# Kernel tuning notes

Measured on AMD Instinct MI355X. Metric: run time of the kernel, lower is better.

## Reference

```python
import jax, jax.numpy as jnp
import numpy as np
from jax import lax


def setup_inputs() -> dict:
    key = jax.random.key(0)
    t_in = jax.random.normal(key, (16, 65536, 3), dtype=jnp.float32)
    return {"npoints": 2048, "t_in": t_in}


def reference(npoints, t_in):
    """Iterative farthest point sampling.

    t_in: (b, n, 3) float32 point coordinates.
    Returns (b, npoints) int32 indices of sampled points.
    Matches the PointNet++ CUDA kernel semantics: first sample is index 0,
    running min-distance buffer initialized to a large value, each step
    picks the argmax of the min-distance to the already-selected set.
    """
    b, n, p = t_in.shape
    assert p == 3
    BIG = jnp.float32(1e10)

    batch_ix = jnp.arange(b)

    def step(carry, _):
        dist, last_idx = carry                      # dist: (b,n), last_idx: (b,)
        last = t_in[batch_ix, last_idx]             # (b,3) last selected points
        d = jnp.sum((t_in - last[:, None, :]) ** 2, axis=-1)  # (b,n)
        dist = jnp.minimum(dist, d)
        nxt = jnp.argmax(dist, axis=-1).astype(jnp.int32)      # (b,)
        return (dist, nxt), nxt

    init_idx = jnp.zeros((b,), dtype=jnp.int32)
    dist0 = jnp.full((b, n), BIG, dtype=jnp.float32)
    (_, _), idxs = lax.scan(step, (dist0, init_idx), None, length=npoints - 1)
    # idxs: (npoints-1, b) -> (b, npoints-1)
    out = jnp.concatenate([init_idx[:, None], idxs.T], axis=1)  # (b, npoints)
    return out
```

## Files before the change

kernel.cpp:

```cpp
#include <hip/hip_runtime.h>
#include <stdint.h>


#define NBATCH   16
#define NPTS     65536
#define NPOINTS  2048
#define KBLK     16
#define THREADS  256
#define PPB      4096
#define PPT      16
#define QPB      4
#define SLOT_U64 2
#define REGION_U64 (KBLK * QPB * SLOT_U64)

#define TAGOK(w) (((unsigned)((w) >> 16) & 0xFFFFu) == tag)

typedef unsigned int uint4v __attribute__((ext_vector_type(4)));
typedef unsigned int uint2v __attribute__((ext_vector_type(2)));

__device__ __forceinline__ void load_slot16(const unsigned long long* p,
                                            unsigned long long& w0,
                                            unsigned long long& w1) {
    uint4v r;
    asm volatile("global_load_dwordx4 %0, %1, off sc1\n\t"
                 "s_waitcnt vmcnt(0)"
                 : "=v"(r) : "v"(p) : "memory");
    w0 = ((unsigned long long)r.y << 32) | r.x;
    w1 = ((unsigned long long)r.w << 32) | r.z;
}

__device__ __forceinline__ void red_combine(double& d, int& i,
                                            double od, int oi) {
    const bool t = (od > d) || (od == d && oi < i);
    d = t ? od : d; i = t ? oi : i;
}

template <int CTRL>
__device__ __forceinline__ void red_dpp(double& d, int& i) {
    const int hi = __double2hiint(d), lo = __double2loint(d);
    const int ohi = __builtin_amdgcn_update_dpp(hi, hi, CTRL, 0xF, 0xF, false);
    const int olo = __builtin_amdgcn_update_dpp(lo, lo, CTRL, 0xF, 0xF, false);
    const int oi  = __builtin_amdgcn_update_dpp(i,  i,  CTRL, 0xF, 0xF, false);
    red_combine(d, i, __hiloint2double(ohi, olo), oi);
}

__device__ __forceinline__ void red_swz16(double& d, int& i) {
    const int ohi = __builtin_amdgcn_ds_swizzle(__double2hiint(d), 0x401F);
    const int olo = __builtin_amdgcn_ds_swizzle(__double2loint(d), 0x401F);
    const int oi  = __builtin_amdgcn_ds_swizzle(i, 0x401F);
    red_combine(d, i, __hiloint2double(ohi, olo), oi);
}

__device__ __forceinline__ void red_x32(double& d, int& i, bool hi_half) {
    const unsigned hi = (unsigned)__double2hiint(d);
    const unsigned lo = (unsigned)__double2loint(d);
    uint2v rh = __builtin_amdgcn_permlane32_swap(hi, hi, false, false);
    uint2v rl = __builtin_amdgcn_permlane32_swap(lo, lo, false, false);
    uint2v ri = __builtin_amdgcn_permlane32_swap((unsigned)i, (unsigned)i,
                                                 false, false);
    const int ohi = (int)(hi_half ? rh[0] : rh[1]);
    const int olo = (int)(hi_half ? rl[0] : rl[1]);
    const int oi  = (int)(hi_half ? ri[0] : ri[1]);
    red_combine(d, i, __hiloint2double(ohi, olo), oi);
}

__device__ __forceinline__ void argmax64(double& d, int& i, bool hi_half) {
    red_dpp<0xB1>(d, i);
    red_dpp<0x4E>(d, i);
    red_dpp<0x141>(d, i);
    red_dpp<0x140>(d, i);
    red_swz16(d, i);
    red_x32(d, i, hi_half);
}

__global__ __launch_bounds__(THREADS, 1)
void fps_kernel(const float* __restrict__ pts, int* __restrict__ out,
                unsigned long long* __restrict__ slots)
{
    const int bid  = blockIdx.x;
    const int g    = bid & 15;
    const int blk  = bid >> 4;
    const int tid  = threadIdx.x;
    const int lane = tid & 63;
    const int wave = tid >> 6;
    const bool hi_half = (lane >= 32);

    const float* __restrict__ P = pts + (size_t)g * (NPTS * 3);

    __shared__ unsigned long long s_mail[2][4];

    double xd[PPT], yd[PPT], zd[PPT], dist[PPT];
    const int base = blk * PPB;
#pragma unroll
    for (int j = 0; j < PPT; ++j) {
        const int idx = base + j * THREADS + tid;
        xd[j] = (double)P[idx * 3 + 0];
        yd[j] = (double)P[idx * 3 + 1];
        zd[j] = (double)P[idx * 3 + 2];
        dist[j] = 1e10;
    }
    if (tid < 8) ((unsigned long long*)s_mail)[tid] = 0ull;
    __syncthreads();

    double qx = (double)P[0], qy = (double)P[1], qz = (double)P[2];
    if (blk == 0 && tid == 0) out[g * NPOINTS] = 0;

    for (int it = 0; it < NPOINTS - 1; ++it) {
        double bd = -1.0;
        int    bi = 0x7FFFFFFF;
        {
#pragma clang fp contract(off)
#pragma unroll
            for (int j = 0; j < PPT; ++j) {
                const double dx = xd[j] - qx;
                const double dy = yd[j] - qy;
                const double dz = zd[j] - qz;
                const double d  = (dx * dx + dy * dy) + dz * dz;
                const double nd = fmin(dist[j], d);
                dist[j] = nd;
                const bool t = nd > bd;
                bd = t ? nd : bd;
                bi = t ? (base + j * THREADS + tid) : bi;
            }
        }

        argmax64(bd, bi, hi_half);

        const unsigned tag = (unsigned)(it + 1);
        const int par = it & 1;
        unsigned long long* rb =
            slots + (size_t)(par * NBATCH + g) * REGION_U64;

        const unsigned long long B =
            (unsigned long long)__double_as_longlong(bd);
        const unsigned long long TI =
              ((unsigned long long)tag << 16)
            | (unsigned long long)((unsigned)bi & 0xFFFFu);
        const unsigned long long own0 = ((B >> 32) << 32) | TI;
        const unsigned long long own1 = ((B & 0xFFFFFFFFull) << 32) | TI;

        if (lane < 2) {
            __hip_atomic_store(rb + (blk * QPB + wave) * SLOT_U64 + lane,
                               (lane == 0) ? own0 : own1,
                               __ATOMIC_RELAXED,
                               __HIP_MEMORY_SCOPE_AGENT);
        }

        float qxf, qyf, qzf;

        if (wave != 0) {
            unsigned long long f1, f2, f3;
            int guard = 0;
            bool okm;
            do {
                f1 = __hip_atomic_load(&s_mail[par][0], __ATOMIC_RELAXED,
                                       __HIP_MEMORY_SCOPE_WORKGROUP);
                f2 = __hip_atomic_load(&s_mail[par][1], __ATOMIC_RELAXED,
                                       __HIP_MEMORY_SCOPE_WORKGROUP);
                f3 = __hip_atomic_load(&s_mail[par][2], __ATOMIC_RELAXED,
                                       __HIP_MEMORY_SCOPE_WORKGROUP);
                okm = ((unsigned)f1 == tag) & ((unsigned)f2 == tag)
                    & ((unsigned)f3 == tag);
            } while (!okm && ++guard < (1 << 20));
            qxf = __int_as_float((int)(f1 >> 32));
            qyf = __int_as_float((int)(f2 >> 32));
            qzf = __int_as_float((int)(f3 >> 32));
        } else {
            unsigned long long* sp = rb + lane * SLOT_U64;
            const bool own = (lane == blk * QPB);
            unsigned long long l0 = own0, l1 = own1;
            bool ok = own;
            __builtin_amdgcn_s_sleep(12);
            int g1 = 0;
            while (!ok && g1 < 32) {
                load_slot16(sp, l0, l1);
                ok = TAGOK(l0) & TAGOK(l1);
                ++g1;
            }
            int g2 = 0;
            while (!ok) {
                l0 = __hip_atomic_load(sp + 0, __ATOMIC_RELAXED,
                                       __HIP_MEMORY_SCOPE_AGENT);
                l1 = __hip_atomic_load(sp + 1, __ATOMIC_RELAXED,
                                       __HIP_MEMORY_SCOPE_AGENT);
                ok = TAGOK(l0) & TAGOK(l1);
                if (++g2 > (1 << 20)) break;
            }

            double cd = __longlong_as_double(
                (long long)(((l0 >> 32) << 32) | (l1 >> 32)));
            int    ci = (int)(l0 & 0xFFFFull);

            const int    si = ci;
            const float* pc = P + (size_t)(unsigned)si * 3;
            const float px = pc[0];
            const float py = pc[1];
            const float pz = pc[2];

            argmax64(cd, ci, hi_half);

            if (lane == 0 && blk == 0) out[g * NPOINTS + it + 1] = ci;

            const unsigned long long mb = __ballot(si == ci);
            const int wl = (__ffsll(mb) - 1) & 63;
            qxf = __int_as_float(
                __builtin_amdgcn_readlane(__float_as_int(px), wl));
            qyf = __int_as_float(
                __builtin_amdgcn_readlane(__float_as_int(py), wl));
            qzf = __int_as_float(
                __builtin_amdgcn_readlane(__float_as_int(pz), wl));

            if (lane < 3) {
                const unsigned coord =
                    (lane == 0) ? (unsigned)__float_as_int(qxf)
                  : (lane == 1) ? (unsigned)__float_as_int(qyf)
                                : (unsigned)__float_as_int(qzf);
                __hip_atomic_store(&s_mail[par][lane],
                                   ((unsigned long long)coord << 32)
                                 | (unsigned long long)tag,
                                   __ATOMIC_RELAXED,
                                   __HIP_MEMORY_SCOPE_WORKGROUP);
            }
        }

        qx = (double)qxf; qy = (double)qyf; qz = (double)qzf;
    }
}

extern "C" void kernel_launch(void* const* d_in, const int* in_sizes, int n_in,
                              void* d_out, int out_size, void* d_ws, size_t ws_size,
                              hipStream_t stream) {
    (void)in_sizes; (void)n_in; (void)out_size; (void)ws_size;
    const float* t_in = (const float*)d_in[1];
    int* out = (int*)d_out;
    unsigned long long* slots = (unsigned long long*)d_ws;

    dim3 grid(NBATCH * KBLK);
    dim3 block(THREADS);
    void* args[] = { (void*)&t_in, (void*)&out, (void*)&slots };
    hipLaunchCooperativeKernel((const void*)fps_kernel, grid, block, args, 0, stream);
}
```

Baseline: 4.301 ms.

## Publish winner coordinates in exchange slots and poll via pipelined global-to-LDS loads

Each wave now tracks the float coordinates of its local best point and publishes them, tag-protected, alongside distance and index in a wider 4-word slot. The exchange wave no longer has to gather the winning point's coordinates from global memory after the cross-block reduction. Polling switches from a serialized load-and-wait loop to four rounds of asynchronous global-to-LDS loads that stay in flight together, and slot writes now use atomic swap instructions. This takes a dependent global load off the per-iteration critical path and shortens polling latency, at the cost of extra registers, LDS buffers and more traffic per slot. The wide path is chosen only when the workspace is large enough, with the old path kept as a fallback.

Result: slower. 7.668 ms (+78.3%).

```diff
diff --git a/kernel.cpp b/kernel.cpp
--- a/kernel.cpp
+++ b/kernel.cpp
@@ -10,23 +10,25 @@
 #define PPB      4096
 #define PPT      16
 #define QPB      4
-#define SLOT_U64 2
-#define REGION_U64 (KBLK * QPB * SLOT_U64)
+#define SLOT_N   2
+#define REGION_N (KBLK * QPB * SLOT_N)
+#define SLOT_W   4
+#define REGION_W (KBLK * QPB * SLOT_W)
+#define WS_NEED_WIDE (2 * NBATCH * REGION_W * 8)
 
 #define TAGOK(w) (((unsigned)((w) >> 16) & 0xFFFFu) == tag)
 
 typedef unsigned int uint4v __attribute__((ext_vector_type(4)));
 typedef unsigned int uint2v __attribute__((ext_vector_type(2)));
-
-__device__ __forceinline__ void load_slot16(const unsigned long long* p,
-                                            unsigned long long& w0,
-                                            unsigned long long& w1) {
+typedef unsigned long long ull;
+
+__device__ __forceinline__ void load_slot16(const ull* p, ull& w0, ull& w1) {
     uint4v r;
     asm volatile("global_load_dwordx4 %0, %1, off sc1\n\t"
                  "s_waitcnt vmcnt(0)"
                  : "=v"(r) : "v"(p) : "memory");
-    w0 = ((unsigned long long)r.y << 32) | r.x;
-    w1 = ((unsigned long long)r.w << 32) | r.z;
+    w0 = ((ull)r.y << 32) | r.x;
+    w1 = ((ull)r.w << 32) | r.z;
 }
 
 __device__ __forceinline__ void red_combine(double& d, int& i,
@@ -73,9 +75,10 @@
     red_x32(d, i, hi_half);
 }
 
+template <int WIDE>
 __global__ __launch_bounds__(THREADS, 1)
 void fps_kernel(const float* __restrict__ pts, int* __restrict__ out,
-                unsigned long long* __restrict__ slots)
+                ull* __restrict__ slots)
 {
     const int bid  = blockIdx.x;
     const int g    = bid & 15;
@@ -87,19 +90,23 @@
 
     const float* __restrict__ P = pts + (size_t)g * (NPTS * 3);
 
-    __shared__ unsigned long long s_mail[2][4];
+    __shared__ ull s_mail[2][4];
+    __shared__ ull pbuf[4][2][64][2];
 
     double xd[PPT], yd[PPT], zd[PPT], dist[PPT];
+    float  xf[PPT], yf[PPT], zf[PPT];
     const int base = blk * PPB;
 #pragma unroll
     for (int j = 0; j < PPT; ++j) {
         const int idx = base + j * THREADS + tid;
-        xd[j] = (double)P[idx * 3 + 0];
-        yd[j] = (double)P[idx * 3 + 1];
-        zd[j] = (double)P[idx * 3 + 2];
+        const float a = P[idx * 3 + 0];
+        const float b = P[idx * 3 + 1];
+        const float c = P[idx * 3 + 2];
+        xd[j] = (double)a; yd[j] = (double)b; zd[j] = (double)c;
+        if (WIDE) { xf[j] = a; yf[j] = b; zf[j] = c; }
         dist[j] = 1e10;
     }
-    if (tid < 8) ((unsigned long long*)s_mail)[tid] = 0ull;
+    if (tid < 8) ((ull*)s_mail)[tid] = 0ull;
     __syncthreads();
 
     double qx = (double)P[0], qy = (double)P[1], qz = (double)P[2];
@@ -108,6 +115,7 @@
     for (int it = 0; it < NPOINTS - 1; ++it) {
         double bd = -1.0;
         int    bi = 0x7FFFFFFF;
+        float  bx = 0.f, by = 0.f, bz = 0.f;
         {
 #pragma clang fp contract(off)
 #pragma unroll
@@ -121,6 +129,11 @@
                 const bool t = nd > bd;
                 bd = t ? nd : bd;
                 bi = t ? (base + j * THREADS + tid) : bi;
+                if (WIDE) {
+                    bx = t ? xf[j] : bx;
+                    by = t ? yf[j] : by;
+                    bz = t ? zf[j] : bz;
+                }
             }
         }
 
@@ -128,28 +141,47 @@
 
         const unsigned tag = (unsigned)(it + 1);
         const int par = it & 1;
-        unsigned long long* rb =
-            slots + (size_t)(par * NBATCH + g) * REGION_U64;
-
-        const unsigned long long B =
-            (unsigned long long)__double_as_longlong(bd);
-        const unsigned long long TI =
-              ((unsigned long long)tag << 16)
-            | (unsigned long long)((unsigned)bi & 0xFFFFu);
-        const unsigned long long own0 = ((B >> 32) << 32) | TI;
-        const unsigned long long own1 = ((B & 0xFFFFFFFFull) << 32) | TI;
-
-        if (lane < 2) {
-            __hip_atomic_store(rb + (blk * QPB + wave) * SLOT_U64 + lane,
-                               (lane == 0) ? own0 : own1,
-                               __ATOMIC_RELAXED,
-                               __HIP_MEMORY_SCOPE_AGENT);
+        ull* rb = slots + (size_t)(par * NBATCH + g)
+                        * (WIDE ? REGION_W : REGION_N);
+
+        const ull B  = (ull)__double_as_longlong(bd);
+        const ull TI = ((ull)tag << 16) | (ull)((unsigned)bi & 0xFFFFu);
+        const ull own0 = ((B >> 32) << 32) | TI;
+        const ull own1 = ((B & 0xFFFFFFFFull) << 32) | TI;
+        ull own2 = 0, own3 = 0;
+        if (WIDE) {
+            const int src_lane = (bi - base) & 63;
+            const unsigned xw = (unsigned)__builtin_amdgcn_readlane(
+                                    __float_as_int(bx), src_lane);
+            const unsigned yw = (unsigned)__builtin_amdgcn_readlane(
+                                    __float_as_int(by), src_lane);
+            const unsigned zw = (unsigned)__builtin_amdgcn_readlane(
+                                    __float_as_int(bz), src_lane);
+            own2 = ((ull)xw << 32) | ((ull)tag << 16) | (ull)(yw >> 16);
+            own3 = ((ull)zw << 32) | ((ull)tag << 16) | (ull)(yw & 0xFFFFu);
         }
 
+        if (WIDE) {
+            if (lane < 4) {
+                ull* dst = rb + (blk * QPB + wave) * SLOT_W + lane;
+                const ull v = (lane == 0) ? own0 : (lane == 1) ? own1
+                            : (lane == 2) ? own2 : own3;
+                asm volatile("global_atomic_swap_x2 %0, %1, off"
+                             :: "v"(dst), "v"(v) : "memory");
+            }
+        } else {
+            if (lane < 2) {
+                ull* dst = rb + (blk * QPB + wave) * SLOT_N + lane;
+                const ull v = (lane == 0) ? own0 : own1;
+                asm volatile("global_atomic_swap_x2 %0, %1, off"
+                             :: "v"(dst), "v"(v) : "memory");
+            }
+        }
+
         float qxf, qyf, qzf;
 
         if (wave != 0) {
-            unsigned long long f1, f2, f3;
+            ull f1, f2, f3;
             int guard = 0;
             bool okm;
             do {
@@ -165,10 +197,109 @@
             qxf = __int_as_float((int)(f1 >> 32));
             qyf = __int_as_float((int)(f2 >> 32));
             qzf = __int_as_float((int)(f3 >> 32));
+        } else if (WIDE) {
+            ull* sp = rb + lane * SLOT_W;
+            const bool own = (lane == blk * QPB);
+            ull l0 = own0, l1 = own1, l2 = own2, l3 = own3;
+            bool ok = own;
+
+#define GLDS(gp, lp)                                                  \
+    __builtin_amdgcn_global_load_lds(                                 \
+        (const __attribute__((address_space(1))) void*)(gp),          \
+        (__attribute__((address_space(3))) void*)(lp), 16, 0, 16)
+
+            __builtin_amdgcn_s_sleep(2);
+            GLDS(sp,     &pbuf[0][0][0][0]);
+            GLDS(sp + 2, &pbuf[0][1][0][0]);
+            __builtin_amdgcn_s_sleep(4);
+            GLDS(sp,     &pbuf[1][0][0][0]);
+            GLDS(sp + 2, &pbuf[1][1][0][0]);
+            __builtin_amdgcn_s_sleep(4);
+            GLDS(sp,     &pbuf[2][0][0][0]);
+            GLDS(sp + 2, &pbuf[2][1][0][0]);
+            __builtin_amdgcn_s_sleep(4);
+            GLDS(sp,     &pbuf[3][0][0][0]);
+            GLDS(sp + 2, &pbuf[3][1][0][0]);
+
+#define CHECKL(r)                                                     \
+    {                                                                 \
+        const ull t0 = pbuf[r][0][lane][0];                           \
+        const ull t1 = pbuf[r][0][lane][1];                           \
+        const ull t2 = pbuf[r][1][lane][0];                           \
+        const ull t3 = pbuf[r][1][lane][1];                           \
+        const bool hit = (!ok) & TAGOK(t0) & TAGOK(t1)                \
+                               & TAGOK(t2) & TAGOK(t3);               \
+        l0 = hit ? t0 : l0; l1 = hit ? t1 : l1;                       \
+        l2 = hit ? t2 : l2; l3 = hit ? t3 : l3;                       \
+        ok |= hit;                                                    \
+    }
+#define PH(r)                                                         \
+    asm volatile("s_waitcnt vmcnt(6)" ::: "memory");                  \
+    __builtin_amdgcn_sched_barrier(0);                                \
+    CHECKL(r);                                                        \
+    allok = __all(ok);                                                \
+    if (allok) break;                                                 \
+    GLDS(sp,     &pbuf[r][0][0][0]);                                  \
+    GLDS(sp + 2, &pbuf[r][1][0][0]);
+
+            int rounds = 0;
+            bool allok = __all(ok);
+            while (!allok && rounds < 64) {
+                PH(0);
+                PH(1);
+                PH(2);
+                PH(3);
+                rounds += 4;
+            }
+            if (!allok) {
+                int g2 = 0;
+                while (!ok) {
+                    l0 = __hip_atomic_load(sp + 0, __ATOMIC_RELAXED,
+                                           __HIP_MEMORY_SCOPE_AGENT);
+                    l1 = __hip_atomic_load(sp + 1, __ATOMIC_RELAXED,
+                                           __HIP_MEMORY_SCOPE_AGENT);
+                    l2 = __hip_atomic_load(sp + 2, __ATOMIC_RELAXED,
+                                           __HIP_MEMORY_SCOPE_AGENT);
+                    l3 = __hip_atomic_load(sp + 3, __ATOMIC_RELAXED,
+                                           __HIP_MEMORY_SCOPE_AGENT);
+                    ok = TAGOK(l0) & TAGOK(l1) & TAGOK(l2) & TAGOK(l3);
+                    if (++g2 > (1 << 20)) break;
+                }
+            }
+
+            double cd = __longlong_as_double(
+                (long long)(((l0 >> 32) << 32) | (l1 >> 32)));
+            int    ci = (int)(l0 & 0xFFFFull);
+            const int si = ci;
+            const unsigned xb = (unsigned)(l2 >> 32);
+            const unsigned zb = (unsigned)(l3 >> 32);
+            const unsigned yb = (((unsigned)l2 & 0xFFFFu) << 16)
+                              |  ((unsigned)l3 & 0xFFFFu);
+
+            argmax64(cd, ci, hi_half);
+
+            if (lane == 0 && blk == 0) out[g * NPOINTS + it + 1] = ci;
+
+            const ull mb = __ballot(si == ci);
+            const int wl = (__ffsll(mb) - 1) & 63;
+            qxf = __int_as_float(__builtin_amdgcn_readlane((int)xb, wl));
+            qyf = __int_as_float(__builtin_amdgcn_readlane((int)yb, wl));
+            qzf = __int_as_float(__builtin_amdgcn_readlane((int)zb, wl));
+
+            if (lane < 3) {
+                const unsigned coord =
+                    (lane == 0) ? (unsigned)__float_as_int(qxf)
+                  : (lane == 1) ? (unsigned)__float_as_int(qyf)
+                                : (unsigned)__float_as_int(qzf);
+                __hip_atomic_store(&s_mail[par][lane],
+                                   ((ull)coord << 32) | (ull)tag,
+                                   __ATOMIC_RELAXED,
+                                   __HIP_MEMORY_SCOPE_WORKGROUP);
+            }
         } else {
-            unsigned long long* sp = rb + lane * SLOT_U64;
+            ull* sp = rb + lane * SLOT_N;
             const bool own = (lane == blk * QPB);
-            unsigned long long l0 = own0, l1 = own1;
+            ull l0 = own0, l1 = own1;
             bool ok = own;
             __builtin_amdgcn_s_sleep(12);
             int g1 = 0;
@@ -201,7 +332,7 @@
 
             if (lane == 0 && blk == 0) out[g * NPOINTS + it + 1] = ci;
 
-            const unsigned long long mb = __ballot(si == ci);
+            const ull mb = __ballot(si == ci);
             const int wl = (__ffsll(mb) - 1) & 63;
             qxf = __int_as_float(
                 __builtin_amdgcn_readlane(__float_as_int(px), wl));
@@ -216,8 +347,7 @@
                   : (lane == 1) ? (unsigned)__float_as_int(qyf)
                                 : (unsigned)__float_as_int(qzf);
                 __hip_atomic_store(&s_mail[par][lane],
-                                   ((unsigned long long)coord << 32)
-                                 | (unsigned long long)tag,
+                                   ((ull)coord << 32) | (ull)tag,
                                    __ATOMIC_RELAXED,
                                    __HIP_MEMORY_SCOPE_WORKGROUP);
             }
@@ -230,13 +360,16 @@
 extern "C" void kernel_launch(void* const* d_in, const int* in_sizes, int n_in,
                               void* d_out, int out_size, void* d_ws, size_t ws_size,
                               hipStream_t stream) {
-    (void)in_sizes; (void)n_in; (void)out_size; (void)ws_size;
+    (void)in_sizes; (void)n_in; (void)out_size;
     const float* t_in = (const float*)d_in[1];
     int* out = (int*)d_out;
-    unsigned long long* slots = (unsigned long long*)d_ws;
+    ull* slots = (ull*)d_ws;
 
     dim3 grid(NBATCH * KBLK);
     dim3 block(THREADS);
     void* args[] = { (void*)&t_in, (void*)&out, (void*)&slots };
-    hipLaunchCooperativeKernel((const void*)fps_kernel, grid, block, args, 0, stream);
-}
+    const void* kfn = (ws_size >= (size_t)WS_NEED_WIDE)
+        ? (const void*)fps_kernel<1>
+        : (const void*)fps_kernel<0>;
+    hipLaunchCooperativeKernel(kfn, grid, block, args, 0, stream);
+}
```
